# Kernel optimization log

Hardware: AMD Instinct MI355X
Metric: run time of the kernel (lower is better)

The kernel has to match this reference:

```python
import jax, jax.numpy as jnp
import numpy as np
import math
from jax import lax

B, C, T = 32, 256, 1024
KS = 64          # key_size
KERN = 3         # conv kernel size
PAD = 2          # (KERN-1)*dilation, chomped -> causal left pad
SQRT_KS = math.sqrt(KS)


def setup_inputs() -> dict:
    key = jax.random.key(0)
    ks = jax.random.split(key, 14)
    s = 0.01
    return {
        "x":  jax.random.normal(ks[0], (B, C, T), jnp.float32),
        # attention linears (stored [in, out])
        "wq": jax.random.normal(ks[1], (C, KS), jnp.float32) * s,
        "bq": jnp.zeros((KS,), jnp.float32),
        "wk": jax.random.normal(ks[2], (C, KS), jnp.float32) * s,
        "bk": jnp.zeros((KS,), jnp.float32),
        "wv": jax.random.normal(ks[3], (C, C), jnp.float32) * s,
        "bv": jnp.zeros((C,), jnp.float32),
        # weight-normed conv 1: v [out,in,k], g [out], b [out]
        "v1": jax.random.normal(ks[4], (C, C, KERN), jnp.float32) * s,
        "g1": jnp.ones((C,), jnp.float32),
        "b1": jnp.zeros((C,), jnp.float32),
        # weight-normed conv 2
        "v2": jax.random.normal(ks[5], (C, C, KERN), jnp.float32) * s,
        "g2": jnp.ones((C,), jnp.float32),
        "b2": jnp.zeros((C,), jnp.float32),
    }


def _wn_conv_relu(h, v, g, b):
    # weight_norm (dim=0): W = g * v / ||v||, norm over (in, k) per out channel
    norm = jnp.sqrt(jnp.sum(v * v, axis=(1, 2), keepdims=True))
    W = (g[:, None, None] / norm) * v
    # left-pad PAD == Conv1d(padding=PAD) + Chomp1d(PAD)  (causal conv)
    y = lax.conv_general_dilated(h, W, window_strides=(1,), padding=[(PAD, 0)],
                                 dimension_numbers=("NCH", "OIH", "NCH"))
    return jax.nn.relu(y + b[None, :, None])


def reference(x, wq, bq, wk, bk, wv, bv, v1, g1, b1, v2, g2, b2):
    t = x.shape[2]
    xt = jnp.swapaxes(x, 1, 2)                      # [B, T, C]
    q = xt @ wq + bq                                # [B, T, KS]
    k = xt @ wk + bk                                # [B, T, KS]
    v = xt @ wv + bv                                # [B, T, C]
    scores = jnp.einsum("bqd,bkd->bqk", q, k)       # [B, Tq, Tk]
    # torch mask[j][i] = 1 if i > j -> masked where key index > query index
    idx = jnp.arange(t)
    mask = idx[None, :] > idx[:, None]              # [Tq, Tk]
    scores = jnp.where(mask[None], -jnp.inf, scores)
    # NOTE: source applies softmax over dim=1 (the QUERY axis) — faithful quirk
    attn = jax.nn.softmax(scores / SQRT_KS, axis=1)  # [B, Tq, Tk]
    out_attn = jnp.einsum("bqk,bkc->bqc", attn, v)  # [B, T, C]
    out_attn = jnp.swapaxes(out_attn, 1, 2)         # [B, C, T]
    # conv stack (dropout=0 / eval)
    out = _wn_conv_relu(out_attn, v1, g1, b1)
    out = _wn_conv_relu(out, v2, g2, b2)
    # en_res branch: per-timestep scaling of x by softmaxed attention mass
    weight_x = jax.nn.softmax(jnp.sum(attn, axis=2), axis=1)  # [B, T]
    en_res_x = weight_x[:, None, :] * x                       # [B, C, T]
    # downsample is None (n_inputs == n_outputs)
    return jax.nn.relu(out + x + en_res_x)
```

## Files before the change

### kernel.cpp

```cpp
#include <hip/hip_runtime.h>
#include <math.h>

#define BB 32
#define CC 256
#define TT 1024

typedef __attribute__((ext_vector_type(4))) float f4;
typedef __attribute__((ext_vector_type(4))) float f32x4;
typedef __attribute__((ext_vector_type(16))) float f32x16;
typedef __attribute__((ext_vector_type(8))) short s8;
typedef __attribute__((ext_vector_type(4))) short s4v;

__device__ inline short f2bf(float f) {
    unsigned u = __builtin_bit_cast(unsigned, f);
    u = (u + 0x7FFFu + ((u >> 16) & 1u)) >> 16;
    return (short)u;
}

static const size_t OFF_QBF  = 0;
static const size_t OFF_KBF  = 4194304;
static const size_t OFF_VT   = 8388608;
static const size_t OFF_OA   = 25165824;
static const size_t OFF_C1   = 58720256;
static const size_t OFF_CRZ  = 75497472;
static const size_t OFF_RS   = 75628544;
static const size_t OFF_WX   = 75759616;
static const size_t OFF_W1   = 75890688;
static const size_t OFF_W2   = 76283904;
static const size_t OFF_WQKV = 76677120;

__global__ __launch_bounds__(256)
void wn_kernel(const float* __restrict__ v1, const float* __restrict__ g1,
               const float* __restrict__ v2, const float* __restrict__ g2,
               short* __restrict__ w1bf, short* __restrict__ w2bf) {
    __shared__ float red[4];
    int which = blockIdx.x >> 8, o = blockIdx.x & 255;
    const float* v = which ? v2 : v1;
    const float* g = which ? g2 : g1;
    short* wt = which ? w2bf : w1bf;
    const float* row = v + (size_t)o * 768;
    int tid = threadIdx.x, lane = tid & 63, wv_ = tid >> 6;
    float r0 = row[tid], r1 = row[tid + 256], r2 = row[tid + 512];
    float s = r0 * r0 + r1 * r1 + r2 * r2;
    for (int d = 1; d < 64; d <<= 1) s += __shfl_xor(s, d, 64);
    if (lane == 0) red[wv_] = s;
    __syncthreads();
    float scale = g[o] * rsqrtf(red[0] + red[1] + red[2] + red[3]);
    for (int j = 0; j < 3; ++j)
        wt[((size_t)(j * 256 + o)) * 256 + tid] = f2bf(scale * row[tid * 3 + j]);
// ... 55 lines not shown
        for (int p = 0; p < 4; ++p) acc[i][j][p] = 0.f;

    for (int kc = 0; kc < 4; ++kc) {
        int c0 = kc * 64;
        __syncthreads();
        for (int it = 0; it < 4; ++it) {
            int idx = tid + 256 * it;
            int row = idx >> 3, seg = idx & 7;
            *reinterpret_cast<s8*>(&Asm[row * 72 + seg * 8]) =
                *reinterpret_cast<const s8*>(&xt[((size_t)b * TT + t0 + row) * CC + c0 + seg * 8]);
        }
        for (int it = 0; it < 2; ++it) {
            int idx = tid + 256 * it;
            int row = idx >> 3, seg = idx & 7;
            *reinterpret_cast<s8*>(&Bsm[row * 72 + seg * 8]) =
                *reinterpret_cast<const s8*>(&wqkv[(size_t)(n0 + row) * 256 + c0 + seg * 8]);
        }
        __syncthreads();
        for (int ks = 0; ks < 2; ++ks)
            for (int mt2 = 0; mt2 < 2; ++mt2) {
                s8 a = *reinterpret_cast<const s8*>(&Asm[(wv_ * 32 + mt2 * 16 + n15) * 72 + quad * 8 + ks * 32]);
                for (int nt = 0; nt < 4; ++nt) {
                    s8 bb = *reinterpret_cast<const s8*>(&Bsm[(nt * 16 + n15) * 72 + quad * 8 + ks * 32]);
                    acc[mt2][nt] = __builtin_amdgcn_mfma_f32_16x16x32_bf16(a, bb, acc[mt2][nt], 0, 0, 0);
                }
            }
    }
    if (n0 < 128) {
        short* outp = (n0 == 0) ? qbf : kbf;
        const float* bias = (n0 == 0) ? bq : bk;
        for (int mt2 = 0; mt2 < 2; ++mt2)
            for (int nt = 0; nt < 4; ++nt) {
                int n_ = nt * 16 + n15;
                float bvl = bias[n_];
                for (int reg = 0; reg < 4; ++reg) {
                    int t = t0 + wv_ * 32 + mt2 * 16 + quad * 4 + reg;
                    outp[((size_t)b * TT + t) * 64 + n_] = f2bf(acc[mt2][nt][reg] + bvl);
                }
            }
    } else {
        int cbase = n0 - 128;
        __syncthreads();
        short* Tw = SL + wv_ * 3072;
        for (int mt2 = 0; mt2 < 2; ++mt2)
            for (int nt = 0; nt < 4; ++nt) {
                int n_ = nt * 16 + n15;
                float bvl = bv[cbase + n_];
                for (int reg = 0; reg < 4; ++reg)
                    Tw[n_ * 48 + mt2 * 16 + quad * 4 + reg] = f2bf(acc[mt2][nt][reg] + bvl);
            }
        for (int p = 0; p < 4; ++p) {
            int n_ = (lane >> 2) + 16 * p;
            int seg = lane & 3;
            s8 vv = *reinterpret_cast<const s8*>(&Tw[n_ * 48 + seg * 8]);
            *reinterpret_cast<s8*>(&vt[((size_t)b * CC + cbase + n_) * TT + t0 + wv_ * 32 + seg * 8]) = vv;
        }
    }
}

__global__ __launch_bounds__(512, 2)
void colz_kernel(const short* __restrict__ qbf, const short* __restrict__ kbf,
                 float* __restrict__ colrz) {
    __shared__ short Qs[64 * 72], Ks[64 * 72];
    __shared__ float redz[8 * 32];
    int tid = threadIdx.x, wv_ = tid >> 6, lane = tid & 63;
    int l31 = lane & 31, lh = lane >> 5;
    int qhalf = wv_ & 1, khalf = (wv_ >> 1) & 1, w4 = wv_ >> 2;
    int b = blockIdx.x & 31, pr = blockIdx.x >> 5;
    int kts[2] = {pr, 15 - pr};
    int row = tid >> 3, sg = (tid & 7) * 8;

    for (int ph = 0; ph < 2; ++ph) {
        int kt = kts[ph];
        s8 kr0 = *reinterpret_cast<const s8*>(&kbf[((size_t)b * TT + kt * 64 + row) * 64 + sg]);
        s8 qr0 = *reinterpret_cast<const s8*>(&qbf[((size_t)b * TT + kt * 64 + row) * 64 + sg]);
        float zloc = 0.f;
        for (int qt = kt; qt < 16; ++qt) {
            __syncthreads();
            if (qt == kt) *reinterpret_cast<s8*>(&Ks[row * 72 + sg]) = kr0;
            *reinterpret_cast<s8*>(&Qs[row * 72 + sg]) = qr0;
            __syncthreads();
            if (qt < 15)
                qr0 = *reinterpret_cast<const s8*>(&qbf[((size_t)b * TT + (qt + 1) * 64 + row) * 64 + sg]);
            f32x16 s;
            for (int p = 0; p < 16; ++p) s[p] = 0.f;
            for (int kc = 0; kc < 4; ++kc) {
                s8 a  = *reinterpret_cast<const s8*>(&Qs[(qhalf * 32 + l31) * 72 + kc * 16 + lh * 8]);
                s8 bb = *reinterpret_cast<const s8*>(&Ks[(khalf * 32 + l31) * 72 + kc * 16 + lh * 8]);
                s = __builtin_amdgcn_mfma_f32_32x32x16_bf16(a, bb, s, 0, 0, 0);
            }
            int kg = kt * 64 + khalf * 32 + l31;
            int qb0 = qt * 64 + qhalf * 32 + 4 * lh;
            if (qt > kt) {
                for (int r = 0; r < 8; ++r) {
                    int reg = w4 * 8 + r;
                    zloc += __expf(s[reg] * 0.125f);
                }
            } else {
                for (int r = 0; r < 8; ++r) {
                    int reg = w4 * 8 + r;
                    if (qb0 + (reg & 3) + 8 * (reg >> 2) >= kg) zloc += __expf(s[reg] * 0.125f);
                }
            }
        }
        float zc = zloc + __shfl_xor(zloc, 32, 64);
        if (lane < 32) redz[wv_ * 32 + lane] = zc;
        __syncthreads();
        if (tid < 64) {
            int kh = tid >> 5, kk = tid & 31;
            float Z;
            if (kh == 0) Z = redz[0 * 32 + kk] + redz[1 * 32 + kk] + redz[4 * 32 + kk] + redz[5 * 32 + kk];
            else         Z = redz[2 * 32 + kk] + redz[3 * 32 + kk] + redz[6 * 32 + kk] + redz[7 * 32 + kk];
            colrz[(size_t)b * TT + kt * 64 + tid] = 1.0f / Z;
        }
        __syncthreads();
    }
}

__global__ __launch_bounds__(512, 2)
void attn_kernel(const short* __restrict__ qbf, const short* __restrict__ kbf,
                 const short* __restrict__ vt, const float* __restrict__ colrz,
                 short* __restrict__ oab, float* __restrict__ rowsum) {
    __shared__ short Qs[64 * 72];
    __shared__ short Ks[64 * 72];
    __shared__ short Ps[64 * 72];
    __shared__ short Vs[256 * 72];
    __shared__ float redR[2][64];
    int tid = threadIdx.x, wv_ = tid >> 6, lane = tid & 63;
    int l31 = lane & 31, lh = lane >> 5;
    int wq2 = wv_ & 1, wk2 = (wv_ >> 1) & 1, w4 = wv_ >> 2, wcq = wv_ >> 1;
    int b = blockIdx.x & 31, pr = blockIdx.x >> 5;
    int qts[2] = {15 - pr, pr};
    int row = tid >> 3, sg = (tid & 7) * 8;

    s8 kreg, vreg[4];
    {
        kreg = *reinterpret_cast<const s8*>(&kbf[((size_t)b * TT + row) * 64 + sg]);
        for (int it = 0; it < 4; ++it) {
            int idx = tid + 512 * it;
            int vr = idx >> 3, seg = idx & 7;
            vreg[it] = *reinterpret_cast<const s8*>(&vt[((size_t)b * CC + vr) * TT + seg * 8]);
        }
    }

    for (int ph = 0; ph < 2; ++ph) {
        int qt = qts[ph];
        s8 qr0 = *reinterpret_cast<const s8*>(&qbf[((size_t)b * TT + qt * 64 + row) * 64 + sg]);
        f32x16 acc[2];
        for (int i = 0; i < 2; ++i) for (int p = 0; p < 16; ++p) acc[i][p] = 0.f;
        float rsum[8];
        for (int i = 0; i < 8; ++i) rsum[i] = 0.f;

        for (int kt = 0; kt <= qt; ++kt) {
            __syncthreads();
            if (kt == 0) *reinterpret_cast<s8*>(&Qs[row * 72 + sg]) = qr0;
            *reinterpret_cast<s8*>(&Ks[row * 72 + sg]) = kreg;
            for (int it = 0; it < 4; ++it) {
                int idx = tid + 512 * it;
                int vr = idx >> 3, seg = idx & 7;
                *reinterpret_cast<s8*>(&Vs[vr * 72 + seg * 8]) = vreg[it];
            }
            __syncthreads();
            int nkt = (kt < qt) ? kt + 1 : ((ph == 0) ? 0 : -1);
            if (nkt >= 0) {
                kreg = *reinterpret_cast<const s8*>(&kbf[((size_t)b * TT + nkt * 64 + row) * 64 + sg]);
                for (int it = 0; it < 4; ++it) {
                    int idx = tid + 512 * it;
                    int vr = idx >> 3, seg = idx & 7;
                    vreg[it] = *reinterpret_cast<const s8*>(&vt[((size_t)b * CC + vr) * TT + nkt * 64 + seg * 8]);
                }
            }
            f32x16 s;
            for (int p = 0; p < 16; ++p) s[p] = 0.f;
            for (int kc = 0; kc < 4; ++kc) {
                s8 a  = *reinterpret_cast<const s8*>(&Qs[(wq2 * 32 + l31) * 72 + kc * 16 + lh * 8]);
                s8 bb = *reinterpret_cast<const s8*>(&Ks[(wk2 * 32 + l31) * 72 + kc * 16 + lh * 8]);
                s = __builtin_amdgcn_mfma_f32_32x32x16_bf16(a, bb, s, 0, 0, 0);
            }
            int kg = kt * 64 + wk2 * 32 + l31;
            float rz = colrz[(size_t)b * TT + kg];
            bool full = (kt < qt);
            int qb0 = qt * 64 + wq2 * 32 + 4 * lh;
            for (int r = 0; r < 8; ++r) {
                int reg = w4 * 8 + r;
                int rr = (reg & 3) + 8 * (reg >> 2);
                float p = 0.f;
                if (full || qb0 + rr >= kg) p = __expf(s[reg] * 0.125f) * rz;
                rsum[r] += p;
                Ps[(wq2 * 32 + rr + 4 * lh) * 72 + wk2 * 32 + l31] = f2bf(p);
            }
            __syncthreads();
            for (int kc = 0; kc < 4; ++kc) {
                s8 a = *reinterpret_cast<const s8*>(&Ps[(wq2 * 32 + l31) * 72 + kc * 16 + lh * 8]);
                for (int nt = 0; nt < 2; ++nt) {
                    s8 bb = *reinterpret_cast<const s8*>(&Vs[(wcq * 64 + nt * 32 + l31) * 72 + kc * 16 + lh * 8]);
                    acc[nt] = __builtin_amdgcn_mfma_f32_32x32x16_bf16(a, bb, acc[nt], 0, 0, 0);
                }
            }
        }
        for (int r = 0; r < 8; ++r) {
            float v = rsum[r];
            v += __shfl_xor(v, 1, 64);
            v += __shfl_xor(v, 2, 64);
            v += __shfl_xor(v, 4, 64);
            v += __shfl_xor(v, 8, 64);
            v += __shfl_xor(v, 16, 64);
            int reg = w4 * 8 + r;
            int rr = (reg & 3) + 8 * (reg >> 2);
            if (l31 == 0) redR[wk2][wq2 * 32 + rr + 4 * lh] = v;
        }
        for (int nt = 0; nt < 2; ++nt) {
            int c = wcq * 64 + nt * 32 + l31;
            for (int reg = 0; reg < 16; ++reg) {
                int q = qt * 64 + wq2 * 32 + (reg & 3) + 8 * (reg >> 2) + 4 * lh;
                oab[((size_t)b * TT + q) * CC + c] = f2bf(acc[nt][reg]);
            }
        }
        __syncthreads();
        if (tid < 64) rowsum[(size_t)b * TT + qt * 64 + tid] = redR[0][tid] + redR[1][tid];
        __syncthreads();
    }
}

__global__ __launch_bounds__(256, 3)
void conv_kernel(const void* __restrict__ inp, int in_is_fp32,
                 const short* __restrict__ wbf, const float* __restrict__ bias,
                 void* __restrict__ outp, int out_is_bf16,
                 const float* __restrict__ xres, const float* __restrict__ wxv,
                 int fuse_final) {
    __shared__ short SL[130 * 72 + 3 * 64 * 72];
    short* As = SL;
    short* Bs = SL + 130 * 72;
    int tid = threadIdx.x, wv_ = tid >> 6, lane = tid & 63;
    int n15 = lane & 15, quad = lane >> 4;
    int bid = blockIdx.x;
    int r = bid & 7;
    int n0 = ((bid >> 3) & 3) << 6;
    int bm = (bid >> 5) * 8 + r;
    int b = bm >> 3, mt = bm & 7;
    int t0 = mt * 128;
    f32x4 acc[2][4];
    for (int i = 0; i < 2; ++i) for (int j = 0; j < 4; ++j)
        for (int p = 0; p < 4; ++p) acc[i][j][p] = 0.f;

    for (int kc = 0; kc < 4; ++kc) {
        int c0 = kc * 64;
        __syncthreads();
        if (in_is_fp32) {
            const float* in = (const float*)inp;
            for (int it = 0; it < 9; ++it) {
                int idx = tid + 256 * it;
                int row = idx >> 4, fc = idx & 15;
                if (row < 130) {
                    int t = t0 + row - 2;
                    s4v st;
                    if (t >= 0) {
                        f4 v = *reinterpret_cast<const f4*>(&in[((size_t)b * TT + t) * CC + c0 + fc * 4]);
                        for (int p = 0; p < 4; ++p) st[p] = f2bf(v[p]);
                    } else { for (int p = 0; p < 4; ++p) st[p] = 0; }
                    *reinterpret_cast<s4v*>(&As[row * 72 + fc * 4]) = st;
                }
            }
        } else {
            const short* in = (const short*)inp;
            for (int it = 0; it < 5; ++it) {
                int idx = tid + 256 * it;
                int row = idx >> 3, seg = idx & 7;
                if (row < 130) {
                    int t = t0 + row - 2;
                    s8 st;
                    if (t >= 0) st = *reinterpret_cast<const s8*>(&in[((size_t)b * TT + t) * CC + c0 + seg * 8]);
                    else for (int p = 0; p < 8; ++p) st[p] = 0;
                    *reinterpret_cast<s8*>(&As[row * 72 + seg * 8]) = st;
                }
            }
        }
        for (int it = 0; it < 6; ++it) {
            int idx = tid + 256 * it;
            int row = idx >> 3, seg = idx & 7;
            int j = row >> 6, o = row & 63;
            *reinterpret_cast<s8*>(&Bs[row * 72 + seg * 8]) =
                *reinterpret_cast<const s8*>(&wbf[((size_t)(j * 256 + n0 + o)) * 256 + c0 + seg * 8]);
        }
        __syncthreads();
        for (int j = 0; j < 3; ++j)
            for (int ks = 0; ks < 2; ++ks)
                for (int mt2 = 0; mt2 < 2; ++mt2) {
                    s8 a = *reinterpret_cast<const s8*>(&As[(wv_ * 32 + mt2 * 16 + n15 + j) * 72 + quad * 8 + ks * 32]);
                    for (int nt = 0; nt < 4; ++nt) {
                        s8 bb = *reinterpret_cast<const s8*>(&Bs[(j * 64 + nt * 16 + n15) * 72 + quad * 8 + ks * 32]);
                        acc[mt2][nt] = __builtin_amdgcn_mfma_f32_16x16x32_bf16(a, bb, acc[mt2][nt], 0, 0, 0);
                    }
                }
    }
    if (!fuse_final) {
        for (int mt2 = 0; mt2 < 2; ++mt2)
            for (int nt = 0; nt < 4; ++nt) {
                int o = n0 + nt * 16 + n15;
                float bvl = bias[o];
                for (int reg = 0; reg < 4; ++reg) {
                    int t = t0 + wv_ * 32 + mt2 * 16 + quad * 4 + reg;
                    float v = fmaxf(acc[mt2][nt][reg] + bvl, 0.f);
                    if (out_is_bf16) ((short*)outp)[((size_t)b * TT + t) * CC + o] = f2bf(v);
                    else             ((float*)outp)[((size_t)b * TT + t) * CC + o] = v;
                }
            }
    } else {
        float* Ft = (float*)SL;
        __syncthreads();
        for (int mt2 = 0; mt2 < 2; ++mt2)
            for (int nt = 0; nt < 4; ++nt) {
                int ol = nt * 16 + n15;
                float bvl = bias[n0 + ol];
                for (int reg = 0; reg < 4; ++reg) {
                    int tl = wv_ * 32 + mt2 * 16 + quad * 4 + reg;
                    Ft[tl * 67 + ol] = fmaxf(acc[mt2][nt][reg] + bvl, 0.f);
                }
            }
        __syncthreads();
        int c_l = tid >> 5;
        int t_l = (tid & 31) * 4;
        f4 wv4 = *reinterpret_cast<const f4*>(&wxv[(size_t)b * TT + t0 + t_l]);
        for (int pass = 0; pass < 8; ++pass) {
            int c = n0 + pass * 8 + c_l;
            f4 xv = *reinterpret_cast<const f4*>(&xres[((size_t)b * CC + c) * TT + t0 + t_l]);
            f4 rr;
            for (int p = 0; p < 4; ++p)
                rr[p] = fmaxf(Ft[(t_l + p) * 67 + pass * 8 + c_l] + xv[p] * (1.f + wv4[p]), 0.f);
            *reinterpret_cast<f4*>(&((float*)outp)[((size_t)b * CC + c) * TT + t0 + t_l]) = rr;
        }
    }
}

__global__ void rowsm_kernel(const float* __restrict__ rowsum, float* __restrict__ wx) {
    __shared__ float red[256];
    int b = blockIdx.x, tid = threadIdx.x;
    float v[4];
    float m = -1e30f;
    for (int r = 0; r < 4; ++r) { v[r] = rowsum[(size_t)b * TT + tid + 256 * r]; m = fmaxf(m, v[r]); }
    red[tid] = m; __syncthreads();
    for (int s = 128; s > 0; s >>= 1) { if (tid < s) red[tid] = fmaxf(red[tid], red[tid + s]); __syncthreads(); }
    m = red[0]; __syncthreads();
    float e[4], zs = 0.f;
    for (int r = 0; r < 4; ++r) { e[r] = __expf(v[r] - m); zs += e[r]; }
    red[tid] = zs; __syncthreads();
    for (int s = 128; s > 0; s >>= 1) { if (tid < s) red[tid] += red[tid + s]; __syncthreads(); }
    float rz = 1.0f / red[0];
    for (int r = 0; r < 4; ++r) wx[(size_t)b * TT + tid + 256 * r] = e[r] * rz;
}

extern "C" void kernel_launch(void* const* d_in, const int* in_sizes, int n_in,
                              void* d_out, int out_size, void* d_ws, size_t ws_size,
                              hipStream_t stream) {
    (void)in_sizes; (void)n_in; (void)out_size; (void)ws_size;
    const float* x  = (const float*)d_in[0];
    const float* wq = (const float*)d_in[1];
    const float* bq = (const float*)d_in[2];
    const float* wk = (const float*)d_in[3];
    const float* bk = (const float*)d_in[4];
    const float* wv = (const float*)d_in[5];
    const float* bv = (const float*)d_in[6];
    const float* v1 = (const float*)d_in[7];
    const float* g1 = (const float*)d_in[8];
    const float* b1 = (const float*)d_in[9];
    const float* v2 = (const float*)d_in[10];
    const float* g2 = (const float*)d_in[11];
    const float* b2 = (const float*)d_in[12];
    char* ws = (char*)d_ws;
    float* out = (float*)d_out;

    short* qbf  = (short*)(ws + OFF_QBF);
    short* kbf  = (short*)(ws + OFF_KBF);
    short* vt   = (short*)(ws + OFF_VT);
    short* xt   = (short*)(ws + OFF_OA);
    short* oab  = (short*)(ws + OFF_OA);
    short* c1   = (short*)(ws + OFF_C1);
    float* crz  = (float*)(ws + OFF_CRZ);
    float* rs   = (float*)(ws + OFF_RS);
    float* wxb  = (float*)(ws + OFF_WX);
    short* w1bf = (short*)(ws + OFF_W1);
    short* w2bf = (short*)(ws + OFF_W2);
    short* wqkv = (short*)(ws + OFF_WQKV);

    wn_kernel<<<dim3(512), dim3(256), 0, stream>>>(v1, g1, v2, g2, w1bf, w2bf);
    pack_kernel<<<dim3(96), dim3(256), 0, stream>>>(wq, wk, wv, wqkv);
    transpose_kernel<<<dim3(4, 16, 32), dim3(256), 0, stream>>>(x, xt);
    qkv_kernel<<<dim3(1536), dim3(256), 0, stream>>>(xt, wqkv, bq, bk, bv, qbf, kbf, vt);
    colz_kernel<<<dim3(256), dim3(512), 0, stream>>>(qbf, kbf, crz);
    attn_kernel<<<dim3(256), dim3(512), 0, stream>>>(qbf, kbf, vt, crz, oab, rs);
    rowsm_kernel<<<dim3(32), dim3(256), 0, stream>>>(rs, wxb);
    conv_kernel<<<dim3(1024), dim3(256), 0, stream>>>(oab, 0, w1bf, b1, c1, 1,
                                                      nullptr, nullptr, 0);
    conv_kernel<<<dim3(1024), dim3(256), 0, stream>>>(c1, 0, w2bf, b2, out, 0,
                                                      x, wxb, 1);
}
```

Baseline: 256.9 us.

## Split attention and column-sum kernels over two key-tile parity halves

Doubles the grid of the column-normaliser and attention kernels by giving each block one parity of tiles (even or odd key/query tiles). Partial column sums, partial row sums and partial attention outputs are written to separate buffers and combined later: in the attention kernel, in rowsm, and in the first conv's input load, which sums the two bf16 halves. This aims to fill more compute units, since 256 blocks underuse the GPU. In exchange it adds an extra bf16 output buffer, extra global traffic, a rounding step when merging the halves, and a launch-bounds change to 4 blocks per SM that may pressure registers.

```diff
diff --git a/kernel.cpp b/kernel.cpp
--- a/kernel.cpp
+++ b/kernel.cpp
@@ -15,6 +15,10 @@
     unsigned u = __builtin_bit_cast(unsigned, f);
     u = (u + 0x7FFFu + ((u >> 16) & 1u)) >> 16;
     return (short)u;
+}
+__device__ inline float bf2f(short s) {
+    unsigned u = ((unsigned)(unsigned short)s) << 16;
+    return __builtin_bit_cast(float, u);
 }
 
 static const size_t OFF_QBF  = 0;
@@ -164,28 +168,33 @@
 
 __global__ __launch_bounds__(512, 2)
 void colz_kernel(const short* __restrict__ qbf, const short* __restrict__ kbf,
-                 float* __restrict__ colrz) {
+                 float* __restrict__ crz0, float* __restrict__ crz1) {
     __shared__ short Qs[64 * 72], Ks[64 * 72];
     __shared__ float redz[8 * 32];
     int tid = threadIdx.x, wv_ = tid >> 6, lane = tid & 63;
     int l31 = lane & 31, lh = lane >> 5;
     int qhalf = wv_ & 1, khalf = (wv_ >> 1) & 1, w4 = wv_ >> 2;
-    int b = blockIdx.x & 31, pr = blockIdx.x >> 5;
+    int bid = blockIdx.x;
+    int b = bid & 31, pr = (bid >> 5) & 7, h = bid >> 8;
     int kts[2] = {pr, 15 - pr};
+    float* zp = h ? crz1 : crz0;
     int row = tid >> 3, sg = (tid & 7) * 8;
 
     for (int ph = 0; ph < 2; ++ph) {
         int kt = kts[ph];
+        int q0 = kt + (((kt & 1) == h) ? 0 : 1);
         s8 kr0 = *reinterpret_cast<const s8*>(&kbf[((size_t)b * TT + kt * 64 + row) * 64 + sg]);
-        s8 qr0 = *reinterpret_cast<const s8*>(&qbf[((size_t)b * TT + kt * 64 + row) * 64 + sg]);
+        s8 qr0;
+        if (q0 < 16)
+            qr0 = *reinterpret_cast<const s8*>(&qbf[((size_t)b * TT + q0 * 64 + row) * 64 + sg]);
         float zloc = 0.f;
-        for (int qt = kt; qt < 16; ++qt) {
+        for (int qt = q0; qt < 16; qt += 2) {
             __syncthreads();
-            if (qt == kt) *reinterpret_cast<s8*>(&Ks[row * 72 + sg]) = kr0;
+            if (qt == q0) *reinterpret_cast<s8*>(&Ks[row * 72 + sg]) = kr0;
             *reinterpret_cast<s8*>(&Qs[row * 72 + sg]) = qr0;
             __syncthreads();
-            if (qt < 15)
-                qr0 = *reinterpret_cast<const s8*>(&qbf[((size_t)b * TT + (qt + 1) * 64 + row) * 64 + sg]);
+            if (qt + 2 < 16)
+                qr0 = *reinterpret_cast<const s8*>(&qbf[((size_t)b * TT + (qt + 2) * 64 + row) * 64 + sg]);
             f32x16 s;
             for (int p = 0; p < 16; ++p) s[p] = 0.f;
             for (int kc = 0; kc < 4; ++kc) {
@@ -215,16 +224,18 @@
             float Z;
             if (kh == 0) Z = redz[0 * 32 + kk] + redz[1 * 32 + kk] + redz[4 * 32 + kk] + redz[5 * 32 + kk];
             else         Z = redz[2 * 32 + kk] + redz[3 * 32 + kk] + redz[6 * 32 + kk] + redz[7 * 32 + kk];
-            colrz[(size_t)b * TT + kt * 64 + tid] = 1.0f / Z;
-        }
-        __syncthreads();
-    }
-}
-
-__global__ __launch_bounds__(512, 2)
+            zp[(size_t)b * TT + kt * 64 + tid] = Z;
+        }
+        __syncthreads();
+    }
+}
+
+__global__ __launch_bounds__(512, 4)
 void attn_kernel(const short* __restrict__ qbf, const short* __restrict__ kbf,
-                 const short* __restrict__ vt, const float* __restrict__ colrz,
-                 short* __restrict__ oab, float* __restrict__ rowsum) {
+                 const short* __restrict__ vt,
+                 const float* __restrict__ crz0, const float* __restrict__ crz1,
+                 short* __restrict__ oab, float* __restrict__ rs0,
+                 float* __restrict__ rs1) {
     __shared__ short Qs[64 * 72];
     __shared__ short Ks[64 * 72];
     __shared__ short Ps[64 * 72];
@@ -233,17 +244,20 @@
     int tid = threadIdx.x, wv_ = tid >> 6, lane = tid & 63;
     int l31 = lane & 31, lh = lane >> 5;
     int wq2 = wv_ & 1, wk2 = (wv_ >> 1) & 1, w4 = wv_ >> 2, wcq = wv_ >> 1;
-    int b = blockIdx.x & 31, pr = blockIdx.x >> 5;
+    int bid = blockIdx.x;
+    int b = bid & 31, pr = (bid >> 5) & 7, h = bid >> 8;
     int qts[2] = {15 - pr, pr};
     int row = tid >> 3, sg = (tid & 7) * 8;
+    short* oabh = oab + (size_t)h * 8388608;
+    float* rsp = h ? rs1 : rs0;
 
     s8 kreg, vreg[4];
     {
-        kreg = *reinterpret_cast<const s8*>(&kbf[((size_t)b * TT + row) * 64 + sg]);
+        kreg = *reinterpret_cast<const s8*>(&kbf[((size_t)b * TT + h * 64 + row) * 64 + sg]);
         for (int it = 0; it < 4; ++it) {
             int idx = tid + 512 * it;
             int vr = idx >> 3, seg = idx & 7;
-            vreg[it] = *reinterpret_cast<const s8*>(&vt[((size_t)b * CC + vr) * TT + seg * 8]);
+            vreg[it] = *reinterpret_cast<const s8*>(&vt[((size_t)b * CC + vr) * TT + h * 64 + seg * 8]);
         }
     }
 
@@ -255,9 +269,9 @@
         float rsum[8];
         for (int i = 0; i < 8; ++i) rsum[i] = 0.f;
 
-        for (int kt = 0; kt <= qt; ++kt) {
+        for (int kt = h; kt <= qt; kt += 2) {
             __syncthreads();
-            if (kt == 0) *reinterpret_cast<s8*>(&Qs[row * 72 + sg]) = qr0;
+            if (kt == h) *reinterpret_cast<s8*>(&Qs[row * 72 + sg]) = qr0;
             *reinterpret_cast<s8*>(&Ks[row * 72 + sg]) = kreg;
             for (int it = 0; it < 4; ++it) {
                 int idx = tid + 512 * it;
@@ -265,7 +279,7 @@
                 *reinterpret_cast<s8*>(&Vs[vr * 72 + seg * 8]) = vreg[it];
             }
             __syncthreads();
-            int nkt = (kt < qt) ? kt + 1 : ((ph == 0) ? 0 : -1);
+            int nkt = (kt + 2 <= qt) ? kt + 2 : ((ph == 0) ? h : -1);
             if (nkt >= 0) {
                 kreg = *reinterpret_cast<const s8*>(&kbf[((size_t)b * TT + nkt * 64 + row) * 64 + sg]);
                 for (int it = 0; it < 4; ++it) {
@@ -282,7 +296,9 @@
                 s = __builtin_amdgcn_mfma_f32_32x32x16_bf16(a, bb, s, 0, 0, 0);
             }
             int kg = kt * 64 + wk2 * 32 + l31;
-            float rz = colrz[(size_t)b * TT + kg];
+            float z0 = crz0[(size_t)b * TT + kg];
+            float z1 = crz1[(size_t)b * TT + kg];
+            float rz = 1.0f / (z0 + z1);
             bool full = (kt < qt);
             int qb0 = qt * 64 + wq2 * 32 + 4 * lh;
             for (int r = 0; r < 8; ++r) {
@@ -317,17 +333,18 @@
             int c = wcq * 64 + nt * 32 + l31;
             for (int reg = 0; reg < 16; ++reg) {
                 int q = qt * 64 + wq2 * 32 + (reg & 3) + 8 * (reg >> 2) + 4 * lh;
-                oab[((size_t)b * TT + q) * CC + c] = f2bf(acc[nt][reg]);
-            }
-        }
-        __syncthreads();
-        if (tid < 64) rowsum[(size_t)b * TT + qt * 64 + tid] = redR[0][tid] + redR[1][tid];
+                oabh[((size_t)b * TT + q) * CC + c] = f2bf(acc[nt][reg]);
+            }
+        }
+        __syncthreads();
+        if (tid < 64) rsp[(size_t)b * TT + qt * 64 + tid] = redR[0][tid] + redR[1][tid];
         __syncthreads();
     }
 }
 
 __global__ __launch_bounds__(256, 3)
-void conv_kernel(const void* __restrict__ inp, int in_is_fp32,
+void conv_kernel(const void* __restrict__ inp, const void* __restrict__ inp2,
+                 int in_is_fp32,
                  const short* __restrict__ wbf, const float* __restrict__ bias,
                  void* __restrict__ outp, int out_is_bf16,
                  const float* __restrict__ xres, const float* __restrict__ wxv,
@@ -367,13 +384,21 @@
             }
         } else {
             const short* in = (const short*)inp;
+            const short* in2 = (const short*)inp2;
             for (int it = 0; it < 5; ++it) {
                 int idx = tid + 256 * it;
                 int row = idx >> 3, seg = idx & 7;
                 if (row < 130) {
                     int t = t0 + row - 2;
                     s8 st;
-                    if (t >= 0) st = *reinterpret_cast<const s8*>(&in[((size_t)b * TT + t) * CC + c0 + seg * 8]);
+                    if (t >= 0) {
+                        st = *reinterpret_cast<const s8*>(&in[((size_t)b * TT + t) * CC + c0 + seg * 8]);
+                        if (in2) {
+                            s8 st2 = *reinterpret_cast<const s8*>(&in2[((size_t)b * TT + t) * CC + c0 + seg * 8]);
+                            for (int p = 0; p < 8; ++p)
+                                st[p] = f2bf(bf2f(st[p]) + bf2f(st2[p]));
+                        }
+                    }
                     else for (int p = 0; p < 8; ++p) st[p] = 0;
                     *reinterpret_cast<s8*>(&As[row * 72 + seg * 8]) = st;
                 }
@@ -436,12 +461,18 @@
     }
 }
 
-__global__ void rowsm_kernel(const float* __restrict__ rowsum, float* __restrict__ wx) {
+__global__ void rowsm_kernel(const float* __restrict__ rs0,
+                             const float* __restrict__ rs1,
+                             float* __restrict__ wx) {
     __shared__ float red[256];
     int b = blockIdx.x, tid = threadIdx.x;
     float v[4];
     float m = -1e30f;
-    for (int r = 0; r < 4; ++r) { v[r] = rowsum[(size_t)b * TT + tid + 256 * r]; m = fmaxf(m, v[r]); }
+    for (int r = 0; r < 4; ++r) {
+        size_t idx = (size_t)b * TT + tid + 256 * r;
+        v[r] = rs0[idx] + rs1[idx];
+        m = fmaxf(m, v[r]);
+    }
     red[tid] = m; __syncthreads();
     for (int s = 128; s > 0; s >>= 1) { if (tid < s) red[tid] = fmaxf(red[tid], red[tid + s]); __syncthreads(); }
     m = red[0]; __syncthreads();
@@ -479,8 +510,10 @@
     short* xt   = (short*)(ws + OFF_OA);
     short* oab  = (short*)(ws + OFF_OA);
     short* c1   = (short*)(ws + OFF_C1);
-    float* crz  = (float*)(ws + OFF_CRZ);
-    float* rs   = (float*)(ws + OFF_RS);
+    float* crz0 = (float*)(ws + OFF_CRZ);
+    float* crz1 = (float*)(ws + OFF_C1 + 131072);
+    float* rs0  = (float*)(ws + OFF_RS);
+    float* rs1  = (float*)(ws + OFF_C1);
     float* wxb  = (float*)(ws + OFF_WX);
     short* w1bf = (short*)(ws + OFF_W1);
     short* w2bf = (short*)(ws + OFF_W2);
@@ -490,11 +523,11 @@
     pack_kernel<<<dim3(96), dim3(256), 0, stream>>>(wq, wk, wv, wqkv);
     transpose_kernel<<<dim3(4, 16, 32), dim3(256), 0, stream>>>(x, xt);
     qkv_kernel<<<dim3(1536), dim3(256), 0, stream>>>(xt, wqkv, bq, bk, bv, qbf, kbf, vt);
-    colz_kernel<<<dim3(256), dim3(512), 0, stream>>>(qbf, kbf, crz);
-    attn_kernel<<<dim3(256), dim3(512), 0, stream>>>(qbf, kbf, vt, crz, oab, rs);
-    rowsm_kernel<<<dim3(32), dim3(256), 0, stream>>>(rs, wxb);
-    conv_kernel<<<dim3(1024), dim3(256), 0, stream>>>(oab, 0, w1bf, b1, c1, 1,
+    colz_kernel<<<dim3(512), dim3(512), 0, stream>>>(qbf, kbf, crz0, crz1);
+    attn_kernel<<<dim3(512), dim3(512), 0, stream>>>(qbf, kbf, vt, crz0, crz1, oab, rs0, rs1);
+    rowsm_kernel<<<dim3(32), dim3(256), 0, stream>>>(rs0, rs1, wxb);
+    conv_kernel<<<dim3(1024), dim3(256), 0, stream>>>(oab, oab + 8388608, 0, w1bf, b1, c1, 1,
                                                       nullptr, nullptr, 0);
-    conv_kernel<<<dim3(1024), dim3(256), 0, stream>>>(c1, 0, w2bf, b2, out, 0,
+    conv_kernel<<<dim3(1024), dim3(256), 0, stream>>>(c1, nullptr, 0, w2bf, b2, out, 0,
                                                       x, wxb, 1);
 }
```

Measured after the change: 287.2 us. 11.8% more time.

## Remove redundant score MFMAs by splitting key tiles across waves

Applied to the files above, without the earlier changes.

Previously every wave recomputed the full 32x32 QK score tile and then used only half of it (8 of 16 registers), so score MFMAs were done twice. In both colz and attn kernels each wave now owns a distinct query/key sub-tile and uses all 16 accumulator registers. colz stages four query tiles per barrier, and attn processes two key tiles per iteration with double K/V/P buffers and Q fragments held in registers. Shared memory and register use grow considerably, which may lower occupancy.

```diff
diff --git a/kernel.cpp b/kernel.cpp
--- a/kernel.cpp
+++ b/kernel.cpp
@@ -165,56 +165,79 @@
 __global__ __launch_bounds__(512, 2)
 void colz_kernel(const short* __restrict__ qbf, const short* __restrict__ kbf,
                  float* __restrict__ colrz) {
-    __shared__ short Qs[64 * 72], Ks[64 * 72];
-    __shared__ float redz[8 * 32];
+    __shared__ short Qs[4][64 * 72];
+    __shared__ short Ks[64 * 72];
+    __shared__ float redz[8][2][32];
     int tid = threadIdx.x, wv_ = tid >> 6, lane = tid & 63;
     int l31 = lane & 31, lh = lane >> 5;
-    int qhalf = wv_ & 1, khalf = (wv_ >> 1) & 1, w4 = wv_ >> 2;
+    int qh = wv_ & 1, ti = wv_ >> 1;
     int b = blockIdx.x & 31, pr = blockIdx.x >> 5;
     int kts[2] = {pr, 15 - pr};
     int row = tid >> 3, sg = (tid & 7) * 8;
 
+    s8 kr = *reinterpret_cast<const s8*>(&kbf[((size_t)b * TT + kts[0] * 64 + row) * 64 + sg]);
+    s8 qreg[4];
+    for (int j = 0; j < 4; ++j) {
+        int t = kts[0] + j; if (t > 15) t = 15;
+        qreg[j] = *reinterpret_cast<const s8*>(&qbf[((size_t)b * TT + t * 64 + row) * 64 + sg]);
+    }
+
     for (int ph = 0; ph < 2; ++ph) {
         int kt = kts[ph];
-        s8 kr0 = *reinterpret_cast<const s8*>(&kbf[((size_t)b * TT + kt * 64 + row) * 64 + sg]);
-        s8 qr0 = *reinterpret_cast<const s8*>(&qbf[((size_t)b * TT + kt * 64 + row) * 64 + sg]);
-        float zloc = 0.f;
-        for (int qt = kt; qt < 16; ++qt) {
+        float zl[2] = {0.f, 0.f};
+        for (int u = kt; u < 16; u += 4) {
             __syncthreads();
-            if (qt == kt) *reinterpret_cast<s8*>(&Ks[row * 72 + sg]) = kr0;
-            *reinterpret_cast<s8*>(&Qs[row * 72 + sg]) = qr0;
+            if (u == kt) *reinterpret_cast<s8*>(&Ks[row * 72 + sg]) = kr;
+            for (int j = 0; j < 4; ++j)
+                *reinterpret_cast<s8*>(&Qs[j][row * 72 + sg]) = qreg[j];
             __syncthreads();
-            if (qt < 15)
-                qr0 = *reinterpret_cast<const s8*>(&qbf[((size_t)b * TT + (qt + 1) * 64 + row) * 64 + sg]);
-            f32x16 s;
-            for (int p = 0; p < 16; ++p) s[p] = 0.f;
-            for (int kc = 0; kc < 4; ++kc) {
-                s8 a  = *reinterpret_cast<const s8*>(&Qs[(qhalf * 32 + l31) * 72 + kc * 16 + lh * 8]);
-                s8 bb = *reinterpret_cast<const s8*>(&Ks[(khalf * 32 + l31) * 72 + kc * 16 + lh * 8]);
-                s = __builtin_amdgcn_mfma_f32_32x32x16_bf16(a, bb, s, 0, 0, 0);
-            }
-            int kg = kt * 64 + khalf * 32 + l31;
-            int qb0 = qt * 64 + qhalf * 32 + 4 * lh;
-            if (qt > kt) {
-                for (int r = 0; r < 8; ++r) {
-                    int reg = w4 * 8 + r;
-                    zloc += __expf(s[reg] * 0.125f);
-                }
-            } else {
-                for (int r = 0; r < 8; ++r) {
-                    int reg = w4 * 8 + r;
-                    if (qb0 + (reg & 3) + 8 * (reg >> 2) >= kg) zloc += __expf(s[reg] * 0.125f);
-                }
-            }
-        }
-        float zc = zloc + __shfl_xor(zloc, 32, 64);
-        if (lane < 32) redz[wv_ * 32 + lane] = zc;
+            int nu = u + 4;
+            if (nu < 16) {
+                for (int j = 0; j < 4; ++j) {
+                    int t = nu + j; if (t > 15) t = 15;
+                    qreg[j] = *reinterpret_cast<const s8*>(&qbf[((size_t)b * TT + t * 64 + row) * 64 + sg]);
+                }
+            } else if (ph == 0) {
+                int k2 = kts[1];
+                kr = *reinterpret_cast<const s8*>(&kbf[((size_t)b * TT + k2 * 64 + row) * 64 + sg]);
+                for (int j = 0; j < 4; ++j) {
+                    int t = k2 + j; if (t > 15) t = 15;
+                    qreg[j] = *reinterpret_cast<const s8*>(&qbf[((size_t)b * TT + t * 64 + row) * 64 + sg]);
+                }
+            }
+            int qtw = u + ti;
+            if (qtw < 16) {
+                for (int kh = 0; kh < 2; ++kh) {
+                    f32x16 s;
+                    for (int p = 0; p < 16; ++p) s[p] = 0.f;
+                    for (int kc = 0; kc < 4; ++kc) {
+                        s8 a  = *reinterpret_cast<const s8*>(&Qs[ti][(qh * 32 + l31) * 72 + kc * 16 + lh * 8]);
+                        s8 bb = *reinterpret_cast<const s8*>(&Ks[(kh * 32 + l31) * 72 + kc * 16 + lh * 8]);
+                        s = __builtin_amdgcn_mfma_f32_32x32x16_bf16(a, bb, s, 0, 0, 0);
+                    }
+                    int kg = kt * 64 + kh * 32 + l31;
+                    int qb0 = qtw * 64 + qh * 32 + 4 * lh;
+                    if (qtw > kt) {
+                        for (int reg = 0; reg < 16; ++reg)
+                            zl[kh] += __expf(s[reg] * 0.125f);
+                    } else {
+                        for (int reg = 0; reg < 16; ++reg) {
+                            int rr = (reg & 3) + 8 * (reg >> 2);
+                            if (qb0 + rr >= kg) zl[kh] += __expf(s[reg] * 0.125f);
+                        }
+                    }
+                }
+            }
+        }
+        for (int kh = 0; kh < 2; ++kh) {
+            float zc = zl[kh] + __shfl_xor(zl[kh], 32, 64);
+            if (lane < 32) redz[wv_][kh][lane] = zc;
+        }
         __syncthreads();
         if (tid < 64) {
             int kh = tid >> 5, kk = tid & 31;
-            float Z;
-            if (kh == 0) Z = redz[0 * 32 + kk] + redz[1 * 32 + kk] + redz[4 * 32 + kk] + redz[5 * 32 + kk];
-            else         Z = redz[2 * 32 + kk] + redz[3 * 32 + kk] + redz[6 * 32 + kk] + redz[7 * 32 + kk];
+            float Z = 0.f;
+            for (int w = 0; w < 8; ++w) Z += redz[w][kh][kk];
             colrz[(size_t)b * TT + kt * 64 + tid] = 1.0f / Z;
         }
         __syncthreads();
@@ -225,93 +248,105 @@
 void attn_kernel(const short* __restrict__ qbf, const short* __restrict__ kbf,
                  const short* __restrict__ vt, const float* __restrict__ colrz,
                  short* __restrict__ oab, float* __restrict__ rowsum) {
-    __shared__ short Qs[64 * 72];
-    __shared__ short Ks[64 * 72];
-    __shared__ short Ps[64 * 72];
-    __shared__ short Vs[256 * 72];
-    __shared__ float redR[2][64];
+    __shared__ short Ks[2][64 * 72];
+    __shared__ short Ps[2][64 * 72];
+    __shared__ short Vs[2][256 * 72];
+    __shared__ float redR[4][64];
     int tid = threadIdx.x, wv_ = tid >> 6, lane = tid & 63;
     int l31 = lane & 31, lh = lane >> 5;
-    int wq2 = wv_ & 1, wk2 = (wv_ >> 1) & 1, w4 = wv_ >> 2, wcq = wv_ >> 1;
+    int wq2 = wv_ & 1;
+    int wk4 = wv_ >> 1;
+    int ksub = wk4 >> 1;
+    int kh2 = wk4 & 1;
+    int wcq = wv_ >> 1;
     int b = blockIdx.x & 31, pr = blockIdx.x >> 5;
     int qts[2] = {15 - pr, pr};
     int row = tid >> 3, sg = (tid & 7) * 8;
 
-    s8 kreg, vreg[4];
-    {
-        kreg = *reinterpret_cast<const s8*>(&kbf[((size_t)b * TT + row) * 64 + sg]);
+    s8 kreg[2], vreg[2][4];
+    for (int j = 0; j < 2; ++j) {
+        kreg[j] = *reinterpret_cast<const s8*>(&kbf[((size_t)b * TT + j * 64 + row) * 64 + sg]);
         for (int it = 0; it < 4; ++it) {
             int idx = tid + 512 * it;
             int vr = idx >> 3, seg = idx & 7;
-            vreg[it] = *reinterpret_cast<const s8*>(&vt[((size_t)b * CC + vr) * TT + seg * 8]);
+            vreg[j][it] = *reinterpret_cast<const s8*>(&vt[((size_t)b * CC + vr) * TT + j * 64 + seg * 8]);
         }
     }
 
     for (int ph = 0; ph < 2; ++ph) {
         int qt = qts[ph];
-        s8 qr0 = *reinterpret_cast<const s8*>(&qbf[((size_t)b * TT + qt * 64 + row) * 64 + sg]);
+        s8 qf[4];
+        for (int kc = 0; kc < 4; ++kc)
+            qf[kc] = *reinterpret_cast<const s8*>(
+                &qbf[((size_t)b * TT + qt * 64 + wq2 * 32 + l31) * 64 + kc * 16 + lh * 8]);
         f32x16 acc[2];
         for (int i = 0; i < 2; ++i) for (int p = 0; p < 16; ++p) acc[i][p] = 0.f;
-        float rsum[8];
-        for (int i = 0; i < 8; ++i) rsum[i] = 0.f;
-
-        for (int kt = 0; kt <= qt; ++kt) {
+        float rsum[16];
+        for (int i = 0; i < 16; ++i) rsum[i] = 0.f;
+
+        for (int kt = 0; kt <= qt; kt += 2) {
+            bool two = (kt + 1 <= qt);
             __syncthreads();
-            if (kt == 0) *reinterpret_cast<s8*>(&Qs[row * 72 + sg]) = qr0;
-            *reinterpret_cast<s8*>(&Ks[row * 72 + sg]) = kreg;
+            *reinterpret_cast<s8*>(&Ks[0][row * 72 + sg]) = kreg[0];
+            if (two) *reinterpret_cast<s8*>(&Ks[1][row * 72 + sg]) = kreg[1];
             for (int it = 0; it < 4; ++it) {
                 int idx = tid + 512 * it;
                 int vr = idx >> 3, seg = idx & 7;
-                *reinterpret_cast<s8*>(&Vs[vr * 72 + seg * 8]) = vreg[it];
+                *reinterpret_cast<s8*>(&Vs[0][vr * 72 + seg * 8]) = vreg[0][it];
+                if (two) *reinterpret_cast<s8*>(&Vs[1][vr * 72 + seg * 8]) = vreg[1][it];
             }
             __syncthreads();
-            int nkt = (kt < qt) ? kt + 1 : ((ph == 0) ? 0 : -1);
+            int nkt = (kt + 2 <= qt) ? kt + 2 : ((ph == 0) ? 0 : -1);
             if (nkt >= 0) {
-                kreg = *reinterpret_cast<const s8*>(&kbf[((size_t)b * TT + nkt * 64 + row) * 64 + sg]);
-                for (int it = 0; it < 4; ++it) {
-                    int idx = tid + 512 * it;
-                    int vr = idx >> 3, seg = idx & 7;
-                    vreg[it] = *reinterpret_cast<const s8*>(&vt[((size_t)b * CC + vr) * TT + nkt * 64 + seg * 8]);
-                }
-            }
-            f32x16 s;
-            for (int p = 0; p < 16; ++p) s[p] = 0.f;
-            for (int kc = 0; kc < 4; ++kc) {
-                s8 a  = *reinterpret_cast<const s8*>(&Qs[(wq2 * 32 + l31) * 72 + kc * 16 + lh * 8]);
-                s8 bb = *reinterpret_cast<const s8*>(&Ks[(wk2 * 32 + l31) * 72 + kc * 16 + lh * 8]);
-                s = __builtin_amdgcn_mfma_f32_32x32x16_bf16(a, bb, s, 0, 0, 0);
-            }
-            int kg = kt * 64 + wk2 * 32 + l31;
-            float rz = colrz[(size_t)b * TT + kg];
-            bool full = (kt < qt);
-            int qb0 = qt * 64 + wq2 * 32 + 4 * lh;
-            for (int r = 0; r < 8; ++r) {
-                int reg = w4 * 8 + r;
-                int rr = (reg & 3) + 8 * (reg >> 2);
-                float p = 0.f;
-                if (full || qb0 + rr >= kg) p = __expf(s[reg] * 0.125f) * rz;
-                rsum[r] += p;
-                Ps[(wq2 * 32 + rr + 4 * lh) * 72 + wk2 * 32 + l31] = f2bf(p);
+                for (int j = 0; j < 2; ++j) {
+                    kreg[j] = *reinterpret_cast<const s8*>(&kbf[((size_t)b * TT + (nkt + j) * 64 + row) * 64 + sg]);
+                    for (int it = 0; it < 4; ++it) {
+                        int idx = tid + 512 * it;
+                        int vr = idx >> 3, seg = idx & 7;
+                        vreg[j][it] = *reinterpret_cast<const s8*>(&vt[((size_t)b * CC + vr) * TT + (nkt + j) * 64 + seg * 8]);
+                    }
+                }
+            }
+            int mykt = kt + ksub;
+            if (two || ksub == 0) {
+                f32x16 s;
+                for (int p = 0; p < 16; ++p) s[p] = 0.f;
+                for (int kc = 0; kc < 4; ++kc) {
+                    s8 bb = *reinterpret_cast<const s8*>(&Ks[ksub][(kh2 * 32 + l31) * 72 + kc * 16 + lh * 8]);
+                    s = __builtin_amdgcn_mfma_f32_32x32x16_bf16(qf[kc], bb, s, 0, 0, 0);
+                }
+                int kg = mykt * 64 + kh2 * 32 + l31;
+                float rz = colrz[(size_t)b * TT + kg];
+                bool full = (mykt < qt);
+                int qb0 = qt * 64 + wq2 * 32 + 4 * lh;
+                for (int reg = 0; reg < 16; ++reg) {
+                    int rr = (reg & 3) + 8 * (reg >> 2);
+                    float p = 0.f;
+                    if (full || qb0 + rr >= kg) p = __expf(s[reg] * 0.125f) * rz;
+                    rsum[reg] += p;
+                    Ps[ksub][(wq2 * 32 + rr + 4 * lh) * 72 + kh2 * 32 + l31] = f2bf(p);
+                }
             }
             __syncthreads();
-            for (int kc = 0; kc < 4; ++kc) {
-                s8 a = *reinterpret_cast<const s8*>(&Ps[(wq2 * 32 + l31) * 72 + kc * 16 + lh * 8]);
-                for (int nt = 0; nt < 2; ++nt) {
-                    s8 bb = *reinterpret_cast<const s8*>(&Vs[(wcq * 64 + nt * 32 + l31) * 72 + kc * 16 + lh * 8]);
-                    acc[nt] = __builtin_amdgcn_mfma_f32_32x32x16_bf16(a, bb, acc[nt], 0, 0, 0);
-                }
-            }
-        }
-        for (int r = 0; r < 8; ++r) {
-            float v = rsum[r];
+            int jmax = two ? 2 : 1;
+            for (int j = 0; j < jmax; ++j)
+                for (int kc = 0; kc < 4; ++kc) {
+                    s8 a = *reinterpret_cast<const s8*>(&Ps[j][(wq2 * 32 + l31) * 72 + kc * 16 + lh * 8]);
+                    for (int nt = 0; nt < 2; ++nt) {
+                        s8 bb = *reinterpret_cast<const s8*>(&Vs[j][(wcq * 64 + nt * 32 + l31) * 72 + kc * 16 + lh * 8]);
+                        acc[nt] = __builtin_amdgcn_mfma_f32_32x32x16_bf16(a, bb, acc[nt], 0, 0, 0);
+                    }
+                }
+        }
+        for (int reg = 0; reg < 16; ++reg) {
+            float v = rsum[reg];
             v += __shfl_xor(v, 1, 64);
             v += __shfl_xor(v, 2, 64);
             v += __shfl_xor(v, 4, 64);
             v += __shfl_xor(v, 8, 64);
             v += __shfl_xor(v, 16, 64);
-            int reg = w4 * 8 + r;
             int rr = (reg & 3) + 8 * (reg >> 2);
-            if (l31 == 0) redR[wk2][wq2 * 32 + rr + 4 * lh] = v;
+            if (l31 == 0) redR[wk4][wq2 * 32 + rr + 4 * lh] = v;
         }
         for (int nt = 0; nt < 2; ++nt) {
             int c = wcq * 64 + nt * 32 + l31;
@@ -321,7 +356,9 @@
             }
         }
         __syncthreads();
-        if (tid < 64) rowsum[(size_t)b * TT + qt * 64 + tid] = redR[0][tid] + redR[1][tid];
+        if (tid < 64)
+            rowsum[(size_t)b * TT + qt * 64 + tid] =
+                redR[0][tid] + redR[1][tid] + redR[2][tid] + redR[3][tid];
         __syncthreads();
     }
 }
```

New measurement: 225.8 us. -12.1%, faster.

## Store Q/K/V in MFMA fragment order and load operands directly to registers

Applied to the files above, without the earlier changes.

The projection kernel now writes Q, K and V^T in a blocked layout that matches the 32x32x16 MFMA operand fragments. The colz and attention kernels load those fragments straight from global memory into registers instead of staging Q/K/V tiles through shared memory. This removes the per-tile LDS writes, reads and barriers. The P tile is double-buffered so only one barrier per key tile remains. The cost is more redundant global/L2 traffic, since each wave loads its own K/V fragments, and more register pressure from holding V fragments.

```diff
diff --git a/kernel.cpp b/kernel.cpp
--- a/kernel.cpp
+++ b/kernel.cpp
@@ -136,10 +136,13 @@
         for (int mt2 = 0; mt2 < 2; ++mt2)
             for (int nt = 0; nt < 4; ++nt) {
                 int n_ = nt * 16 + n15;
+                int kc = n_ >> 4, lhh = (n_ >> 3) & 1, j = n_ & 7;
                 float bvl = bias[n_];
                 for (int reg = 0; reg < 4; ++reg) {
                     int t = t0 + wv_ * 32 + mt2 * 16 + quad * 4 + reg;
-                    outp[((size_t)b * TT + t) * 64 + n_] = f2bf(acc[mt2][nt][reg] + bvl);
+                    int tt = t >> 6, th = (t >> 5) & 1, tl = t & 31;
+                    size_t idx = ((((((size_t)b * 16 + tt) * 2 + th) * 4 + kc) * 2 + lhh) * 32 + tl) * 8 + j;
+                    outp[idx] = f2bf(acc[mt2][nt][reg] + bvl);
                 }
             }
     } else {
@@ -157,7 +160,12 @@
             int n_ = (lane >> 2) + 16 * p;
             int seg = lane & 3;
             s8 vv = *reinterpret_cast<const s8*>(&Tw[n_ * 48 + seg * 8]);
-            *reinterpret_cast<s8*>(&vt[((size_t)b * CC + cbase + n_) * TT + t0 + wv_ * 32 + seg * 8]) = vv;
+            int c = cbase + n_;
+            int t = t0 + wv_ * 32 + seg * 8;
+            int kt = t >> 6, tl = t & 63;
+            int kc = tl >> 4, lhh = (tl >> 3) & 1;
+            size_t idx = ((((((size_t)b * 16 + kt) * 8 + (c >> 5)) * 4 + kc) * 2 + lhh) * 32 + (c & 31)) * 8;
+            *reinterpret_cast<s8*>(&vt[idx]) = vv;
         }
     }
 }
@@ -165,47 +173,44 @@
 __global__ __launch_bounds__(512, 2)
 void colz_kernel(const short* __restrict__ qbf, const short* __restrict__ kbf,
                  float* __restrict__ colrz) {
-    __shared__ short Qs[64 * 72], Ks[64 * 72];
     __shared__ float redz[8 * 32];
     int tid = threadIdx.x, wv_ = tid >> 6, lane = tid & 63;
     int l31 = lane & 31, lh = lane >> 5;
-    int qhalf = wv_ & 1, khalf = (wv_ >> 1) & 1, w4 = wv_ >> 2;
+    int qhf = wv_ & 1, khalf = (wv_ >> 1) & 1, w4 = wv_ >> 2;
     int b = blockIdx.x & 31, pr = blockIdx.x >> 5;
     int kts[2] = {pr, 15 - pr};
-    int row = tid >> 3, sg = (tid & 7) * 8;
 
     for (int ph = 0; ph < 2; ++ph) {
         int kt = kts[ph];
-        s8 kr0 = *reinterpret_cast<const s8*>(&kbf[((size_t)b * TT + kt * 64 + row) * 64 + sg]);
-        s8 qr0 = *reinterpret_cast<const s8*>(&qbf[((size_t)b * TT + kt * 64 + row) * 64 + sg]);
+        s8 kf[4], qf[4], qfn[4];
+        for (int kc = 0; kc < 4; ++kc)
+            kf[kc] = *reinterpret_cast<const s8*>(
+                &kbf[((((((size_t)b * 16 + kt) * 2 + khalf) * 4 + kc) * 2 + lh) * 32 + l31) * 8]);
+        for (int kc = 0; kc < 4; ++kc)
+            qf[kc] = *reinterpret_cast<const s8*>(
+                &qbf[((((((size_t)b * 16 + kt) * 2 + qhf) * 4 + kc) * 2 + lh) * 32 + l31) * 8]);
         float zloc = 0.f;
+        int kg = kt * 64 + khalf * 32 + l31;
         for (int qt = kt; qt < 16; ++qt) {
-            __syncthreads();
-            if (qt == kt) *reinterpret_cast<s8*>(&Ks[row * 72 + sg]) = kr0;
-            *reinterpret_cast<s8*>(&Qs[row * 72 + sg]) = qr0;
-            __syncthreads();
             if (qt < 15)
-                qr0 = *reinterpret_cast<const s8*>(&qbf[((size_t)b * TT + (qt + 1) * 64 + row) * 64 + sg]);
+                for (int kc = 0; kc < 4; ++kc)
+                    qfn[kc] = *reinterpret_cast<const s8*>(
+                        &qbf[((((((size_t)b * 16 + qt + 1) * 2 + qhf) * 4 + kc) * 2 + lh) * 32 + l31) * 8]);
             f32x16 s;
             for (int p = 0; p < 16; ++p) s[p] = 0.f;
-            for (int kc = 0; kc < 4; ++kc) {
-                s8 a  = *reinterpret_cast<const s8*>(&Qs[(qhalf * 32 + l31) * 72 + kc * 16 + lh * 8]);
-                s8 bb = *reinterpret_cast<const s8*>(&Ks[(khalf * 32 + l31) * 72 + kc * 16 + lh * 8]);
-                s = __builtin_amdgcn_mfma_f32_32x32x16_bf16(a, bb, s, 0, 0, 0);
-            }
-            int kg = kt * 64 + khalf * 32 + l31;
-            int qb0 = qt * 64 + qhalf * 32 + 4 * lh;
+            for (int kc = 0; kc < 4; ++kc)
+                s = __builtin_amdgcn_mfma_f32_32x32x16_bf16(qf[kc], kf[kc], s, 0, 0, 0);
+            int qb0 = qt * 64 + qhf * 32 + 4 * lh;
             if (qt > kt) {
-                for (int r = 0; r < 8; ++r) {
-                    int reg = w4 * 8 + r;
-                    zloc += __expf(s[reg] * 0.125f);
-                }
+                for (int r = 0; r < 8; ++r)
+                    zloc += __expf(s[w4 * 8 + r] * 0.125f);
             } else {
                 for (int r = 0; r < 8; ++r) {
                     int reg = w4 * 8 + r;
                     if (qb0 + (reg & 3) + 8 * (reg >> 2) >= kg) zloc += __expf(s[reg] * 0.125f);
                 }
             }
+            for (int kc = 0; kc < 4; ++kc) qf[kc] = qfn[kc];
         }
         float zc = zloc + __shfl_xor(zloc, 32, 64);
         if (lane < 32) redz[wv_ * 32 + lane] = zc;
@@ -225,82 +230,67 @@
 void attn_kernel(const short* __restrict__ qbf, const short* __restrict__ kbf,
                  const short* __restrict__ vt, const float* __restrict__ colrz,
                  short* __restrict__ oab, float* __restrict__ rowsum) {
-    __shared__ short Qs[64 * 72];
-    __shared__ short Ks[64 * 72];
-    __shared__ short Ps[64 * 72];
-    __shared__ short Vs[256 * 72];
+    __shared__ short Ps[2][64 * 72];
     __shared__ float redR[2][64];
     int tid = threadIdx.x, wv_ = tid >> 6, lane = tid & 63;
     int l31 = lane & 31, lh = lane >> 5;
     int wq2 = wv_ & 1, wk2 = (wv_ >> 1) & 1, w4 = wv_ >> 2, wcq = wv_ >> 1;
     int b = blockIdx.x & 31, pr = blockIdx.x >> 5;
     int qts[2] = {15 - pr, pr};
-    int row = tid >> 3, sg = (tid & 7) * 8;
-
-    s8 kreg, vreg[4];
-    {
-        kreg = *reinterpret_cast<const s8*>(&kbf[((size_t)b * TT + row) * 64 + sg]);
-        for (int it = 0; it < 4; ++it) {
-            int idx = tid + 512 * it;
-            int vr = idx >> 3, seg = idx & 7;
-            vreg[it] = *reinterpret_cast<const s8*>(&vt[((size_t)b * CC + vr) * TT + seg * 8]);
-        }
-    }
-
+
+    s8 kf[4], kfn[4], vf[8];
+    for (int kc = 0; kc < 4; ++kc)
+        kf[kc] = *reinterpret_cast<const s8*>(
+            &kbf[((((((size_t)b * 16 + 0) * 2 + wk2) * 4 + kc) * 2 + lh) * 32 + l31) * 8]);
+    int pp = 0;
     for (int ph = 0; ph < 2; ++ph) {
         int qt = qts[ph];
-        s8 qr0 = *reinterpret_cast<const s8*>(&qbf[((size_t)b * TT + qt * 64 + row) * 64 + sg]);
+        s8 qf[4];
+        for (int kc = 0; kc < 4; ++kc)
+            qf[kc] = *reinterpret_cast<const s8*>(
+                &qbf[((((((size_t)b * 16 + qt) * 2 + wq2) * 4 + kc) * 2 + lh) * 32 + l31) * 8]);
         f32x16 acc[2];
         for (int i = 0; i < 2; ++i) for (int p = 0; p < 16; ++p) acc[i][p] = 0.f;
         float rsum[8];
         for (int i = 0; i < 8; ++i) rsum[i] = 0.f;
 
         for (int kt = 0; kt <= qt; ++kt) {
-            __syncthreads();
-            if (kt == 0) *reinterpret_cast<s8*>(&Qs[row * 72 + sg]) = qr0;
-            *reinterpret_cast<s8*>(&Ks[row * 72 + sg]) = kreg;
-            for (int it = 0; it < 4; ++it) {
-                int idx = tid + 512 * it;
-                int vr = idx >> 3, seg = idx & 7;
-                *reinterpret_cast<s8*>(&Vs[vr * 72 + seg * 8]) = vreg[it];
-            }
-            __syncthreads();
-            int nkt = (kt < qt) ? kt + 1 : ((ph == 0) ? 0 : -1);
-            if (nkt >= 0) {
-                kreg = *reinterpret_cast<const s8*>(&kbf[((size_t)b * TT + nkt * 64 + row) * 64 + sg]);
-                for (int it = 0; it < 4; ++it) {
-                    int idx = tid + 512 * it;
-                    int vr = idx >> 3, seg = idx & 7;
-                    vreg[it] = *reinterpret_cast<const s8*>(&vt[((size_t)b * CC + vr) * TT + nkt * 64 + seg * 8]);
-                }
-            }
+            for (int nt = 0; nt < 2; ++nt)
+                for (int kc = 0; kc < 4; ++kc)
+                    vf[nt * 4 + kc] = *reinterpret_cast<const s8*>(
+                        &vt[((((((size_t)b * 16 + kt) * 8 + (wcq * 2 + nt)) * 4 + kc) * 2 + lh) * 32 + l31) * 8]);
             f32x16 s;
             for (int p = 0; p < 16; ++p) s[p] = 0.f;
-            for (int kc = 0; kc < 4; ++kc) {
-                s8 a  = *reinterpret_cast<const s8*>(&Qs[(wq2 * 32 + l31) * 72 + kc * 16 + lh * 8]);
-                s8 bb = *reinterpret_cast<const s8*>(&Ks[(wk2 * 32 + l31) * 72 + kc * 16 + lh * 8]);
-                s = __builtin_amdgcn_mfma_f32_32x32x16_bf16(a, bb, s, 0, 0, 0);
-            }
+            for (int kc = 0; kc < 4; ++kc)
+                s = __builtin_amdgcn_mfma_f32_32x32x16_bf16(qf[kc], kf[kc], s, 0, 0, 0);
+            int nkt = (kt < qt) ? kt + 1 : ((ph == 0) ? 0 : -1);
+            if (nkt >= 0)
+                for (int kc = 0; kc < 4; ++kc)
+                    kfn[kc] = *reinterpret_cast<const s8*>(
+                        &kbf[((((((size_t)b * 16 + nkt) * 2 + wk2) * 4 + kc) * 2 + lh) * 32 + l31) * 8]);
             int kg = kt * 64 + wk2 * 32 + l31;
             float rz = colrz[(size_t)b * TT + kg];
             bool full = (kt < qt);
             int qb0 = qt * 64 + wq2 * 32 + 4 * lh;
+            short* Pw = Ps[pp];
             for (int r = 0; r < 8; ++r) {
                 int reg = w4 * 8 + r;
                 int rr = (reg & 3) + 8 * (reg >> 2);
                 float p = 0.f;
                 if (full || qb0 + rr >= kg) p = __expf(s[reg] * 0.125f) * rz;
                 rsum[r] += p;
-                Ps[(wq2 * 32 + rr + 4 * lh) * 72 + wk2 * 32 + l31] = f2bf(p);
+                Pw[(wq2 * 32 + rr + 4 * lh) * 72 + wk2 * 32 + l31] = f2bf(p);
             }
             __syncthreads();
+            const short* Pr = Ps[pp];
             for (int kc = 0; kc < 4; ++kc) {
-                s8 a = *reinterpret_cast<const s8*>(&Ps[(wq2 * 32 + l31) * 72 + kc * 16 + lh * 8]);
-                for (int nt = 0; nt < 2; ++nt) {
-                    s8 bb = *reinterpret_cast<const s8*>(&Vs[(wcq * 64 + nt * 32 + l31) * 72 + kc * 16 + lh * 8]);
-                    acc[nt] = __builtin_amdgcn_mfma_f32_32x32x16_bf16(a, bb, acc[nt], 0, 0, 0);
-                }
-            }
+                s8 a = *reinterpret_cast<const s8*>(&Pr[(wq2 * 32 + l31) * 72 + kc * 16 + lh * 8]);
+                for (int nt = 0; nt < 2; ++nt)
+                    acc[nt] = __builtin_amdgcn_mfma_f32_32x32x16_bf16(a, vf[nt * 4 + kc], acc[nt], 0, 0, 0);
+            }
+            if (nkt >= 0)
+                for (int kc = 0; kc < 4; ++kc) kf[kc] = kfn[kc];
+            pp ^= 1;
         }
         for (int r = 0; r < 8; ++r) {
             float v = rsum[r];
```

Measured after the change: 274.8 us. 1.07x slower.
